# Kernel optimization log

Hardware: AMD Instinct MI355X
Metric: run time of the kernel (lower is better)

Reference implementation:

```python
import jax, jax.numpy as jnp
import numpy as np

CORR_THRESHOLD = 0.5
EPS = 1e-12


def setup_inputs() -> dict:
    key = jax.random.key(0)
    # x: [B, N_channels, T] EEG windows
    x = jax.random.normal(key, (128, 64, 30720), dtype=jnp.float32)
    return {"x": x}


def reference(x):
    # Batched Pearson correlation across channels (rows = variables, like np.corrcoef).
    B, N, T = x.shape
    xc = x - jnp.mean(x, axis=-1, keepdims=True)            # center over time
    cov = jnp.einsum("bnt,bmt->bnm", xc, xc)                # [B, N, N] unnormalized
    norms = jnp.sqrt(jnp.einsum("bnt,bnt->bn", xc, xc))     # [B, N] row L2 norms
    corr = cov / (norms[:, :, None] * norms[:, None, :] + EPS)
    # zero diagonal, then threshold on |corr|
    eye = jnp.eye(N, dtype=bool)
    corr = jnp.where(eye[None], 0.0, corr)
    mask = jnp.abs(corr) >= CORR_THRESHOLD
    adj = jnp.where(mask, corr, 0.0)                        # dense masked adjacency [B, N, N]
    # node features are the raw EEG samples (as in the original Data(x=eeg_sample, ...))
    return adj, x
```

## Files before the change

### kernel.cpp

```cpp
#include <hip/hip_runtime.h>
#include <hip/hip_bf16.h>
#include <cstdint>
#include <cstddef>

#define B_   128
#define NCH  64
#define T_   30720
#define EPSF 1e-12f
#define THRF 0.5f

typedef float  f32x4 __attribute__((ext_vector_type(4)));
typedef short  s16x8 __attribute__((ext_vector_type(8)));
typedef unsigned short u16;

static __device__ __forceinline__ short bf16s(float f) {
    return (short)__builtin_bit_cast(u16, __float2bfloat16(f));
}

static constexpr int FI[10] = {0,0,0,0,1,1,1,2,2,3};
static constexpr int FJ[10] = {0,1,2,3,1,2,3,2,3,3};

__global__ __launch_bounds__(256) void corr_stage1(
    const float* __restrict__ x, float* __restrict__ out_x,
    float* __restrict__ P, float* __restrict__ S,
    int split, int Tc)
{
    __shared__ float mbuf[4][2560];
    __shared__ float sbuf[4][64];

    const int tid  = threadIdx.x;
    const int lane = tid & 63;
    const int w    = tid >> 6;
    const int cc   = lane & 15;
    const int g    = lane >> 4;

    const int bid = blockIdx.x;
    const int b   = bid / split;
    const int c   = bid - b * split;

    const int NK  = Tc >> 7;
    const int tw0 = w * (Tc >> 2);

    const size_t base = (size_t)b * ((size_t)NCH * T_) + (size_t)c * Tc
                      + (size_t)tw0 + (size_t)(g * 8);
    const float* xw = x + base;
    float*       ow = out_x + base;

    f32x4 acc[10];
    #pragma unroll
    for (int f = 0; f < 10; ++f) acc[f] = (f32x4)(0.f);
    float ssum[4] = {0.f, 0.f, 0.f, 0.f};

    f32x4 L0[4], H0[4], L1[4], H1[4];

    auto ISSUE = [&](int s, f32x4* L, f32x4* H) {
        const int toff = s * 32;
        #pragma unroll
        for (int i = 0; i < 4; ++i) {
            const float* p = xw + (size_t)(i * 16 + cc) * T_ + toff;
            L[i] = *reinterpret_cast<const f32x4*>(p);
            H[i] = *reinterpret_cast<const f32x4*>(p + 4);
        }
    };
    auto CONSUME = [&](int s, f32x4* L, f32x4* H) {
        const int toff = s * 32;
        s16x8 A[4];
        #pragma unroll
        for (int i = 0; i < 4; ++i) {
            float* q = ow + (size_t)(i * 16 + cc) * T_ + toff;
            __builtin_nontemporal_store(L[i], reinterpret_cast<f32x4*>(q));
            __builtin_nontemporal_store(H[i], reinterpret_cast<f32x4*>(q + 4));
            ssum[i] += ((L[i].x + L[i].y) + (L[i].z + L[i].w))
                     + ((H[i].x + H[i].y) + (H[i].z + H[i].w));
            A[i][0] = bf16s(L[i].x); A[i][1] = bf16s(L[i].y);
            A[i][2] = bf16s(L[i].z); A[i][3] = bf16s(L[i].w);
            A[i][4] = bf16s(H[i].x); A[i][5] = bf16s(H[i].y);
            A[i][6] = bf16s(H[i].z); A[i][7] = bf16s(H[i].w);
        }
        #pragma unroll
        for (int f = 0; f < 10; ++f)
            acc[f] = __builtin_amdgcn_mfma_f32_16x16x32_bf16(
                A[FI[f]], A[FJ[f]], acc[f], 0, 0, 0);
    };

    ISSUE(0, L0, H0);
    ISSUE(1, L1, H1);
    for (int s = 0; s < NK; s += 2) {
        CONSUME(s, L0, H0);
        if (s + 2 < NK) ISSUE(s + 2, L0, H0);
        CONSUME(s + 1, L1, H1);
        if (s + 3 < NK) ISSUE(s + 3, L1, H1);
    }

    #pragma unroll
    for (int i = 0; i < 4; ++i) {
        ssum[i] += __shfl_xor(ssum[i], 16, 64);
        ssum[i] += __shfl_xor(ssum[i], 32, 64);
    }
    if (lane < 16) {
        #pragma unroll
        for (int i = 0; i < 4; ++i) sbuf[w][i * 16 + lane] = ssum[i];
    }

    #pragma unroll
    for (int f = 0; f < 10; ++f)
        *reinterpret_cast<f32x4*>(&mbuf[w][f * 256 + lane * 4]) = acc[f];
    __syncthreads();

    float* Pc = P + ((size_t)bid << 12);
    const int l2  = tid >> 2;
    const int rg  = tid & 3;
    const int row = ((l2 >> 4) << 2) + rg;
    const int col = l2 & 15;
    #pragma unroll
    for (int f = 0; f < 10; ++f) {
        const int e = f * 256 + tid;
        const float v = mbuf[0][e] + mbuf[1][e] + mbuf[2][e] + mbuf[3][e];
        const int i = FI[f], j = FJ[f];
        Pc[(i * 16 + row) * 64 + (j * 16 + col)] = v;
        if (i != j)
            Pc[(j * 16 + col) * 64 + (i * 16 + row)] = v;
    }
    if (tid < NCH) {
        const float s = sbuf[0][tid] + sbuf[1][tid] + sbuf[2][tid] + sbuf[3][tid];
        S[(size_t)bid * NCH + tid] = s;
    }
}

__global__ __launch_bounds__(256) void corr_stage2(
    const float* __restrict__ P, const float* __restrict__ S,
    float* __restrict__ adj, int split)
{
    const int idx = blockIdx.x * 256 + threadIdx.x;
    const int b  = idx >> 12;
    const int nm = idx & 4095;
    const int n  = nm >> 6;
    const int m  = nm & 63;

    float G = 0.f, Gnn = 0.f, Gmm = 0.f, Sn = 0.f, Sm = 0.f;
    for (int c = 0; c < split; ++c) {
        const float* Pc = P + ((size_t)(b * split + c) << 12);
        const float* Sc = S + (size_t)(b * split + c) * NCH;
        G   += Pc[nm];
        Gnn += Pc[n * 65];
        Gmm += Pc[m * 65];
        Sn  += Sc[n];
        Sm  += Sc[m];
    }
    const float invT = 1.0f / (float)T_;
    const float cov  = G   - Sn * Sm * invT;
    const float vn   = Gnn - Sn * Sn * invT;
    const float vm   = Gmm - Sm * Sm * invT;
    const float den  = sqrtf(vn) * sqrtf(vm) + EPSF;
    float corr = cov / den;
    if (n == m) corr = 0.f;
    adj[idx] = (fabsf(corr) >= THRF) ? corr : 0.f;
}

extern "C" void kernel_launch(void* const* d_in, const int* in_sizes, int n_in,
                              void* d_out, int out_size, void* d_ws, size_t ws_size,
                              hipStream_t stream)
{
    const float* x   = (const float*)d_in[0];
    float* out   = (float*)d_out;
    float* adj   = out;
    float* out_x = out + (size_t)B_ * NCH * NCH;

    int split = 12;
    while (split > 3 &&
           (size_t)B_ * split * (4096 + NCH) * sizeof(float) > ws_size)
        split >>= 1;

    float* P = (float*)d_ws;
    float* S = P + (size_t)B_ * split * 4096;
    const int Tc = T_ / split;

    corr_stage1<<<dim3(B_ * split), dim3(256), 0, stream>>>(x, out_x, P, S, split, Tc);
    corr_stage2<<<dim3((B_ * 4096) / 256), dim3(256), 0, stream>>>(P, S, adj, split);
}
```

Before: 539.6 us.

## Specialize waves: copy-and-sum waves separate from MFMA Gram waves

Splits each block into two roles. Two wavefronts stream the raw samples to the output copy and accumulate per-channel sums. The other two wavefronts each load the full 64-channel tile again and compute half of the ten 16x16 Gram blocks with bf16 MFMA. This removes the LDS reduction and the __syncthreads, and it also halves the split count and adds a launch-bounds occupancy hint. In exchange, x is read twice per block (once by the copy waves and once by the MFMA waves), which adds global/L2 traffic, and each MFMA wave now covers the whole time chunk on its own.

New measurement: 755.9 us. 40.1% more time.

```diff
diff --git a/kernel.cpp b/kernel.cpp
--- a/kernel.cpp
+++ b/kernel.cpp
@@ -17,113 +17,127 @@
     return (short)__builtin_bit_cast(u16, __float2bfloat16(f));
 }
 
-static constexpr int FI[10] = {0,0,0,0,1,1,1,2,2,3};
-static constexpr int FJ[10] = {0,1,2,3,1,2,3,2,3,3};
-
-__global__ __launch_bounds__(256) void corr_stage1(
+__global__ __launch_bounds__(256, 3) void corr_stage1(
     const float* __restrict__ x, float* __restrict__ out_x,
     float* __restrict__ P, float* __restrict__ S,
     int split, int Tc)
 {
-    __shared__ float mbuf[4][2560];
-    __shared__ float sbuf[4][64];
-
     const int tid  = threadIdx.x;
     const int lane = tid & 63;
     const int w    = tid >> 6;
-    const int cc   = lane & 15;
-    const int g    = lane >> 4;
 
     const int bid = blockIdx.x;
     const int b   = bid / split;
     const int c   = bid - b * split;
 
-    const int NK  = Tc >> 7;
-    const int tw0 = w * (Tc >> 2);
+    const size_t base = (size_t)b * ((size_t)NCH * T_) + (size_t)c * Tc;
 
-    const size_t base = (size_t)b * ((size_t)NCH * T_) + (size_t)c * Tc
-                      + (size_t)tw0 + (size_t)(g * 8);
-    const float* xw = x + base;
-    float*       ow = out_x + base;
+    if (w < 2) {
+        const int ch0 = w * 32;
+        float ssum[32];
+        #pragma unroll
+        for (int i = 0; i < 32; ++i) ssum[i] = 0.f;
 
-    f32x4 acc[10];
-    #pragma unroll
-    for (int f = 0; f < 10; ++f) acc[f] = (f32x4)(0.f);
-    float ssum[4] = {0.f, 0.f, 0.f, 0.f};
+        const int nkt = Tc >> 8;
+        const float* xb = x     + base + (size_t)ch0 * T_ + (size_t)(lane * 4);
+        float*       ob = out_x + base + (size_t)ch0 * T_ + (size_t)(lane * 4);
 
-    f32x4 L0[4], H0[4], L1[4], H1[4];
-
-    auto ISSUE = [&](int s, f32x4* L, f32x4* H) {
-        const int toff = s * 32;
-        #pragma unroll
-        for (int i = 0; i < 4; ++i) {
-            const float* p = xw + (size_t)(i * 16 + cc) * T_ + toff;
-            L[i] = *reinterpret_cast<const f32x4*>(p);
-            H[i] = *reinterpret_cast<const f32x4*>(p + 4);
-        }
-    };
-    auto CONSUME = [&](int s, f32x4* L, f32x4* H) {
-        const int toff = s * 32;
-        s16x8 A[4];
-        #pragma unroll
-        for (int i = 0; i < 4; ++i) {
-            float* q = ow + (size_t)(i * 16 + cc) * T_ + toff;
-            __builtin_nontemporal_store(L[i], reinterpret_cast<f32x4*>(q));
-            __builtin_nontemporal_store(H[i], reinterpret_cast<f32x4*>(q + 4));
-            ssum[i] += ((L[i].x + L[i].y) + (L[i].z + L[i].w))
-                     + ((H[i].x + H[i].y) + (H[i].z + H[i].w));
-            A[i][0] = bf16s(L[i].x); A[i][1] = bf16s(L[i].y);
-            A[i][2] = bf16s(L[i].z); A[i][3] = bf16s(L[i].w);
-            A[i][4] = bf16s(H[i].x); A[i][5] = bf16s(H[i].y);
-            A[i][6] = bf16s(H[i].z); A[i][7] = bf16s(H[i].w);
+        for (int kt = 0; kt < nkt; ++kt) {
+            const int toff = kt * 256;
+            #pragma unroll
+            for (int ch = 0; ch < 32; ++ch) {
+                const size_t o = (size_t)ch * T_ + toff;
+                const f32x4 v = *reinterpret_cast<const f32x4*>(xb + o);
+                __builtin_nontemporal_store(v, reinterpret_cast<f32x4*>(ob + o));
+                ssum[ch] += ((v.x + v.y) + (v.z + v.w));
+            }
         }
         #pragma unroll
-        for (int f = 0; f < 10; ++f)
-            acc[f] = __builtin_amdgcn_mfma_f32_16x16x32_bf16(
-                A[FI[f]], A[FJ[f]], acc[f], 0, 0, 0);
-    };
+        for (int ch = 0; ch < 32; ++ch) {
+            float v = ssum[ch];
+            v += __shfl_xor(v, 1,  64);
+            v += __shfl_xor(v, 2,  64);
+            v += __shfl_xor(v, 4,  64);
+            v += __shfl_xor(v, 8,  64);
+            v += __shfl_xor(v, 16, 64);
+            v += __shfl_xor(v, 32, 64);
+            if (lane == 0) S[(size_t)bid * NCH + ch0 + ch] = v;
+        }
+    } else {
+        const int cw = w - 2;
+        const int cc = lane & 15;
+        const int g  = lane >> 4;
 
-    ISSUE(0, L0, H0);
-    ISSUE(1, L1, H1);
-    for (int s = 0; s < NK; s += 2) {
-        CONSUME(s, L0, H0);
-        if (s + 2 < NK) ISSUE(s + 2, L0, H0);
-        CONSUME(s + 1, L1, H1);
-        if (s + 3 < NK) ISSUE(s + 3, L1, H1);
-    }
+        const float* xw = x + base + (size_t)(g * 8);
+        const int NK = Tc >> 5;
 
-    #pragma unroll
-    for (int i = 0; i < 4; ++i) {
-        ssum[i] += __shfl_xor(ssum[i], 16, 64);
-        ssum[i] += __shfl_xor(ssum[i], 32, 64);
-    }
-    if (lane < 16) {
+        f32x4 acc[5];
         #pragma unroll
-        for (int i = 0; i < 4; ++i) sbuf[w][i * 16 + lane] = ssum[i];
-    }
+        for (int f = 0; f < 5; ++f) acc[f] = (f32x4)(0.f);
 
-    #pragma unroll
-    for (int f = 0; f < 10; ++f)
-        *reinterpret_cast<f32x4*>(&mbuf[w][f * 256 + lane * 4]) = acc[f];
-    __syncthreads();
+        f32x4 L0[4], H0[4], L1[4], H1[4];
 
-    float* Pc = P + ((size_t)bid << 12);
-    const int l2  = tid >> 2;
-    const int rg  = tid & 3;
-    const int row = ((l2 >> 4) << 2) + rg;
-    const int col = l2 & 15;
-    #pragma unroll
-    for (int f = 0; f < 10; ++f) {
-        const int e = f * 256 + tid;
-        const float v = mbuf[0][e] + mbuf[1][e] + mbuf[2][e] + mbuf[3][e];
-        const int i = FI[f], j = FJ[f];
-        Pc[(i * 16 + row) * 64 + (j * 16 + col)] = v;
-        if (i != j)
-            Pc[(j * 16 + col) * 64 + (i * 16 + row)] = v;
-    }
-    if (tid < NCH) {
-        const float s = sbuf[0][tid] + sbuf[1][tid] + sbuf[2][tid] + sbuf[3][tid];
-        S[(size_t)bid * NCH + tid] = s;
+        auto ISSUE = [&](int s, f32x4* L, f32x4* H) {
+            const int toff = s * 32;
+            #pragma unroll
+            for (int i = 0; i < 4; ++i) {
+                const float* p = xw + (size_t)(i * 16 + cc) * T_ + toff;
+                L[i] = *reinterpret_cast<const f32x4*>(p);
+                H[i] = *reinterpret_cast<const f32x4*>(p + 4);
+            }
+        };
+        auto CONSUME = [&](f32x4* L, f32x4* H) {
+            s16x8 A[4];
+            #pragma unroll
+            for (int i = 0; i < 4; ++i) {
+                A[i][0] = bf16s(L[i].x); A[i][1] = bf16s(L[i].y);
+                A[i][2] = bf16s(L[i].z); A[i][3] = bf16s(L[i].w);
+                A[i][4] = bf16s(H[i].x); A[i][5] = bf16s(H[i].y);
+                A[i][6] = bf16s(H[i].z); A[i][7] = bf16s(H[i].w);
+            }
+            if (cw == 0) {
+                acc[0] = __builtin_amdgcn_mfma_f32_16x16x32_bf16(A[0], A[0], acc[0], 0, 0, 0);
+                acc[1] = __builtin_amdgcn_mfma_f32_16x16x32_bf16(A[0], A[1], acc[1], 0, 0, 0);
+                acc[2] = __builtin_amdgcn_mfma_f32_16x16x32_bf16(A[0], A[2], acc[2], 0, 0, 0);
+                acc[3] = __builtin_amdgcn_mfma_f32_16x16x32_bf16(A[0], A[3], acc[3], 0, 0, 0);
+                acc[4] = __builtin_amdgcn_mfma_f32_16x16x32_bf16(A[1], A[1], acc[4], 0, 0, 0);
+            } else {
+                acc[0] = __builtin_amdgcn_mfma_f32_16x16x32_bf16(A[1], A[2], acc[0], 0, 0, 0);
+                acc[1] = __builtin_amdgcn_mfma_f32_16x16x32_bf16(A[1], A[3], acc[1], 0, 0, 0);
+                acc[2] = __builtin_amdgcn_mfma_f32_16x16x32_bf16(A[2], A[2], acc[2], 0, 0, 0);
+                acc[3] = __builtin_amdgcn_mfma_f32_16x16x32_bf16(A[2], A[3], acc[3], 0, 0, 0);
+                acc[4] = __builtin_amdgcn_mfma_f32_16x16x32_bf16(A[3], A[3], acc[4], 0, 0, 0);
+            }
+        };
+
+        ISSUE(0, L0, H0);
+        ISSUE(1, L1, H1);
+        for (int s = 0; s < NK; s += 2) {
+            CONSUME(L0, H0);
+            if (s + 2 < NK) ISSUE(s + 2, L0, H0);
+            CONSUME(L1, H1);
+            if (s + 3 < NK) ISSUE(s + 3, L1, H1);
+        }
+
+        float* Pc = P + ((size_t)bid << 12);
+        const int row = (lane >> 4) << 2;
+        const int col = lane & 15;
+        auto WR = [&](int i, int j, const f32x4& a) {
+            #pragma unroll
+            for (int reg = 0; reg < 4; ++reg) {
+                const float v = a[reg];
+                Pc[(i * 16 + row + reg) * 64 + (j * 16 + col)] = v;
+                if (i != j)
+                    Pc[(j * 16 + col) * 64 + (i * 16 + row + reg)] = v;
+            }
+        };
+        if (cw == 0) {
+            WR(0, 0, acc[0]); WR(0, 1, acc[1]); WR(0, 2, acc[2]);
+            WR(0, 3, acc[3]); WR(1, 1, acc[4]);
+        } else {
+            WR(1, 2, acc[0]); WR(1, 3, acc[1]); WR(2, 2, acc[2]);
+            WR(2, 3, acc[3]); WR(3, 3, acc[4]);
+        }
     }
 }
 
@@ -166,7 +180,7 @@
     float* adj   = out;
     float* out_x = out + (size_t)B_ * NCH * NCH;
 
-    int split = 12;
+    int split = 6;
     while (split > 3 &&
            (size_t)B_ * split * (4096 + NCH) * sizeof(float) > ws_size)
         split >>= 1;
```
